# Kernel tuning notes

Measured on AMD Instinct MI355X. Metric: run time of the kernel, lower is better.

Reference implementation:

```python
import jax, jax.numpy as jnp
import numpy as np
from jax import lax

SEQ, BATCH, D_IN, HID = 2048, 16, 512, 512


def _qrnn_dir(X, W, b):
    # X: [S, B, D]; W: [3H, D]; b: [3H]
    g = jnp.einsum('sbd,hd->sbh', X, W) + b            # [S, B, 3H]
    z, f, o = jnp.split(g, 3, axis=-1)
    z = jnp.tanh(z)
    f = jax.nn.sigmoid(f)
    o = jax.nn.sigmoid(o)
    # fo-pooling recurrence: h_t = f_t*z_t + (1-f_t)*h_{t-1}, h_0 = 0
    # linear recurrence h_t = a_t*h_{t-1} + c_t with a = 1-f, c = f*z
    a = 1.0 - f
    c = f * z

    def combine(e1, e2):
        a1, c1 = e1
        a2, c2 = e2
        return (a1 * a2, a2 * c1 + c2)

    _, h = lax.associative_scan(combine, (a, c), axis=0)
    return o * h                                        # [S, B, H]


def setup_inputs() -> dict:
    key = jax.random.key(0)
    k = jax.random.split(key, 5)
    scale = 0.02
    return {
        'X': jax.random.normal(k[0], (SEQ, BATCH, D_IN), dtype=jnp.float32),
        'W_fw': jax.random.normal(k[1], (3 * HID, D_IN), dtype=jnp.float32) * scale,
        'b_fw': jnp.zeros((3 * HID,), dtype=jnp.float32),
        'W_bw': jax.random.normal(k[2], (3 * HID, D_IN), dtype=jnp.float32) * scale,
        'b_bw': jnp.zeros((3 * HID,), dtype=jnp.float32),
    }


def reference(X, W_fw, b_fw, W_bw, b_bw):
    Yfw = _qrnn_dir(X, W_fw, b_fw)                       # [S, B, H]
    Ybw = _qrnn_dir(jnp.flip(X, axis=0), W_bw, b_bw)     # [S, B, H]
    return jnp.concatenate((Yfw, jnp.flip(Ybw, axis=0)), axis=2)  # [S, B, 2H]
```

## Files before the change

kernel.cpp:

```cpp
#include <hip/hip_runtime.h>
#include <hip/hip_bf16.h>

#define SEQ   2048
#define BATCH 16
#define DIN   512
#define HID   512
#define MROWS (SEQ*BATCH)
#define NCOLS (6*HID)
#define KDIM  DIN

#define NC   32
#define CL   64
#define NSEQ (2*BATCH*HID)

typedef unsigned short u16;
typedef __bf16 bf16x8 __attribute__((ext_vector_type(8)));
typedef float  f32x4  __attribute__((ext_vector_type(4)));

__device__ __forceinline__ u16 f2bf(float x) {
  unsigned u = __float_as_uint(x);
  unsigned r = (u + 0x7fffu + ((u >> 16) & 1u)) >> 16;
  return (u16)r;
}
__device__ __forceinline__ float bflo(unsigned u) { return __uint_as_float(u << 16); }
__device__ __forceinline__ float bfhi(unsigned u) { return __uint_as_float(u & 0xffff0000u); }

__device__ __forceinline__ void async_ld16(const void* g, void* l) {
  __builtin_amdgcn_global_load_lds(
      (const __attribute__((address_space(1))) void*)g,
      (__attribute__((address_space(3))) void*)l, 16, 0, 0);
}

__device__ __forceinline__ float sig_fast(float x) {
  return __builtin_amdgcn_rcpf(1.f + __expf(-x));
}
__device__ __forceinline__ float tanh_fast(float x) {
  return 1.f - 2.f * __builtin_amdgcn_rcpf(1.f + __expf(2.f * x));
}

__global__ void cvt_kernel(const float* __restrict__ in, u16* __restrict__ out, int n4) {
  int i = blockIdx.x * blockDim.x + threadIdx.x;
  if (i >= n4) return;
  const float4 v = ((const float4*)in)[i];
  uint2 r;
  r.x = (unsigned)f2bf(v.x) | ((unsigned)f2bf(v.y) << 16);
  r.y = (unsigned)f2bf(v.z) | ((unsigned)f2bf(v.w) << 16);
  ((uint2*)out)[i] = r;
}

__launch_bounds__(256)
__global__ void gemm_gates(const u16* __restrict__ A, const u16* __restrict__ B,
                           const float* __restrict__ bfw, const float* __restrict__ bbw,
                           u16* __restrict__ G)
{
  __shared__ u16 sA[128 * 32];
  __shared__ u16 sB[128 * 32];

  const int t    = threadIdx.x;
  const int wave = t >> 6;
  const int lane = t & 63;
  const int m0 = blockIdx.y * 128;
  const int n0 = blockIdx.x * 128;
  const int wm = (wave >> 1) * 64;
  const int wn = (wave & 1) * 64;

  f32x4 acc[4][4] = {};

  const int srow = t >> 2;
  const int skcol = ((t & 3) ^ ((t >> 3) & 3)) * 8;
  const u16* gA = A + (size_t)(m0 + srow) * KDIM + skcol;
  const u16* gB = B + (size_t)(n0 + srow) * KDIM + skcol;
  u16* lA0 = sA + wave * 512;
  u16* lA1 = sA + 2048 + wave * 512;
  u16* lB0 = sB + wave * 512;
  u16* lB1 = sB + 2048 + wave * 512;

  const int lm  = lane & 15;
  const int q   = lane >> 4;
  const int swz = (lm >> 1) & 3;
  const int koff = ((q ^ swz) * 8);

  for (int kt = 0; kt < KDIM; kt += 32) {
    __syncthreads();
    async_ld16(gA + kt, lA0);
    async_ld16(gA + kt + (size_t)64 * KDIM, lA1);
    async_ld16(gB + kt, lB0);
    async_ld16(gB + kt + (size_t)64 * KDIM, lB1);
    __syncthreads();

    bf16x8 af[4], bfr[4];
#pragma unroll
    for (int mi = 0; mi < 4; mi++)
      af[mi] = *(const bf16x8*)(sA + (wm + mi * 16 + lm) * 32 + koff);
#pragma unroll
    for (int ni = 0; ni < 4; ni++)
      bfr[ni] = *(const bf16x8*)(sB + (wn + ni * 16 + lm) * 32 + koff);
#pragma unroll
    for (int mi = 0; mi < 4; mi++)
#pragma unroll
      for (int ni = 0; ni < 4; ni++)
        acc[mi][ni] = __builtin_amdgcn_mfma_f32_16x16x32_bf16(bfr[ni], af[mi], acc[mi][ni], 0, 0, 0);
  }

  const int q4 = q * 4;
#pragma unroll
  for (int ni = 0; ni < 4; ni++) {
    const int colb = n0 + wn + ni * 16 + q4;
    const int dir  = colb >= 1536 ? 1 : 0;
    const int rem  = colb - dir * 1536;
    const int gate = rem >> 9;
    const int hb   = rem & 511;
    const float4 bias4 = *(const float4*)((dir ? bbw : bfw) + rem);
    u16* Gs = G + (size_t)(dir * 3 + gate) * MROWS * HID + hb;
#pragma unroll
    for (int mi = 0; mi < 4; mi++) {
      const int m = m0 + wm + mi * 16 + lm;
      float v0 = acc[mi][ni][0] + bias4.x;
      float v1 = acc[mi][ni][1] + bias4.y;
      float v2 = acc[mi][ni][2] + bias4.z;
      float v3 = acc[mi][ni][3] + bias4.w;
      if (gate == 0) {
        v0 = tanh_fast(v0); v1 = tanh_fast(v1); v2 = tanh_fast(v2); v3 = tanh_fast(v3);
      } else {
        v0 = sig_fast(v0); v1 = sig_fast(v1); v2 = sig_fast(v2); v3 = sig_fast(v3);
      }
      uint2 pk;
      pk.x = (unsigned)f2bf(v0) | ((unsigned)f2bf(v1) << 16);
      pk.y = (unsigned)f2bf(v2) | ((unsigned)f2bf(v3) << 16);
      *(uint2*)(Gs + (size_t)m * HID) = pk;
    }
  }
}

__global__ void scan_stage1(const u16* __restrict__ G, float* __restrict__ AC) {
  const int tid = blockIdx.x * 256 + threadIdx.x;
  const int h     = (tid & 127) * 4;
  const int chunk = (tid >> 7) & 31;
  const int b     = (tid >> 12) & 15;
  const int dir   = tid >> 16;
  const u16* Zp = G + (size_t)(dir * 3 + 0) * MROWS * HID;
  const u16* Fp = G + (size_t)(dir * 3 + 1) * MROWS * HID;
  float A0 = 1.f, A1 = 1.f, A2 = 1.f, A3 = 1.f;
  float C0 = 0.f, C1 = 0.f, C2 = 0.f, C3 = 0.f;
  const int tbase = chunk * CL;
  for (int i = 0; i < CL; i++) {
    const int ts = tbase + i;
    const int s = dir ? (SEQ - 1 - ts) : ts;
    const size_t off = ((size_t)s * BATCH + b) * HID + h;
    const uint2 zu = *(const uint2*)(Zp + off);
    const uint2 fu = *(const uint2*)(Fp + off);
    const float z0 = bflo(zu.x), z1 = bfhi(zu.x), z2 = bflo(zu.y), z3 = bfhi(zu.y);
    const float f0 = bflo(fu.x), f1 = bfhi(fu.x), f2 = bflo(fu.y), f3 = bfhi(fu.y);
    const float a0 = 1.f - f0, a1 = 1.f - f1, a2 = 1.f - f2, a3 = 1.f - f3;
    C0 = fmaf(a0, C0, f0 * z0); A0 *= a0;
    C1 = fmaf(a1, C1, f1 * z1); A1 *= a1;
    C2 = fmaf(a2, C2, f2 * z2); A2 *= a2;
    C3 = fmaf(a3, C3, f3 * z3); A3 *= a3;
  }
  const int sidx = (dir * BATCH + b) * HID + h;
  *(float4*)&AC[(size_t)chunk * (2 * NSEQ) + sidx]        = make_float4(A0, A1, A2, A3);
  *(float4*)&AC[(size_t)chunk * (2 * NSEQ) + NSEQ + sidx] = make_float4(C0, C1, C2, C3);
}

__global__ void scan_stage2(const float* __restrict__ AC, float* __restrict__ Hin) {
  const int sidx = blockIdx.x * 256 + threadIdx.x;
  float carry = 0.f;
  for (int chunk = 0; chunk < NC; chunk++) {
    Hin[(size_t)chunk * NSEQ + sidx] = carry;
    const float Aa = AC[(size_t)chunk * (2 * NSEQ) + sidx];
    const float Cc = AC[(size_t)chunk * (2 * NSEQ) + NSEQ + sidx];
    carry = fmaf(Aa, carry, Cc);
  }
}

__global__ void scan_stage3(const u16* __restrict__ G, const float* __restrict__ Hin,
                            float* __restrict__ out) {
  const int tid = blockIdx.x * 256 + threadIdx.x;
  const int h     = (tid & 127) * 4;
  const int chunk = (tid >> 7) & 31;
  const int b     = (tid >> 12) & 15;
  const int dir   = tid >> 16;
  const u16* Zp = G + (size_t)(dir * 3 + 0) * MROWS * HID;
  const u16* Fp = G + (size_t)(dir * 3 + 1) * MROWS * HID;
  const u16* Op = G + (size_t)(dir * 3 + 2) * MROWS * HID;
  const int sidx = (dir * BATCH + b) * HID + h;
  float4 hv = *(const float4*)&Hin[(size_t)chunk * NSEQ + sidx];
  const int tbase = chunk * CL;
  for (int i = 0; i < CL; i++) {
    const int ts = tbase + i;
    const int s = dir ? (SEQ - 1 - ts) : ts;
    const size_t off = ((size_t)s * BATCH + b) * HID + h;
    const uint2 zu = *(const uint2*)(Zp + off);
    const uint2 fu = *(const uint2*)(Fp + off);
    const uint2 ou = *(const uint2*)(Op + off);
    const float z0 = bflo(zu.x), z1 = bfhi(zu.x), z2 = bflo(zu.y), z3 = bfhi(zu.y);
    const float f0 = bflo(fu.x), f1 = bfhi(fu.x), f2 = bflo(fu.y), f3 = bfhi(fu.y);
    hv.x = fmaf(f0, z0 - hv.x, hv.x);
    hv.y = fmaf(f1, z1 - hv.y, hv.y);
    hv.z = fmaf(f2, z2 - hv.z, hv.z);
    hv.w = fmaf(f3, z3 - hv.w, hv.w);
    float4 ov;
    ov.x = bflo(ou.x) * hv.x;
    ov.y = bfhi(ou.x) * hv.y;
    ov.z = bflo(ou.y) * hv.z;
    ov.w = bfhi(ou.y) * hv.w;
    *(float4*)&out[((size_t)s * BATCH + b) * (2 * HID) + (size_t)dir * HID + h] = ov;
  }
}

extern "C" void kernel_launch(void* const* d_in, const int* in_sizes, int n_in,
                              void* d_out, int out_size, void* d_ws, size_t ws_size,
                              hipStream_t stream) {
  const float* X   = (const float*)d_in[0];
  const float* Wfw = (const float*)d_in[1];
  const float* bfw = (const float*)d_in[2];
  const float* Wbw = (const float*)d_in[3];
  const float* bbw = (const float*)d_in[4];
  float* out = (float*)d_out;

  char* ws = (char*)d_ws;
  u16*   Xb  = (u16*)ws;
  u16*   Wb  = (u16*)(ws + (size_t)MROWS * KDIM * 2);
  u16*   G   = (u16*)(ws + (size_t)MROWS * KDIM * 2 + (size_t)NCOLS * KDIM * 2);
  float* AC  = (float*)((char*)G + (size_t)6 * MROWS * HID * 2);
  float* Hin = (float*)((char*)AC + (size_t)NC * 2 * NSEQ * 4);

  cvt_kernel<<<(MROWS * KDIM / 4) / 256, 256, 0, stream>>>(X, Xb, MROWS * KDIM / 4);
  cvt_kernel<<<(3 * HID * KDIM / 4) / 256, 256, 0, stream>>>(Wfw, Wb, 3 * HID * KDIM / 4);
  cvt_kernel<<<(3 * HID * KDIM / 4) / 256, 256, 0, stream>>>(Wbw, Wb + (size_t)3 * HID * KDIM,
                                                             3 * HID * KDIM / 4);

  dim3 gg(NCOLS / 128, MROWS / 128);
  gemm_gates<<<gg, 256, 0, stream>>>(Xb, Wb, bfw, bbw, G);

  scan_stage1<<<(NSEQ * NC / 4) / 256, 256, 0, stream>>>(G, AC);
  scan_stage2<<<NSEQ / 256, 256, 0, stream>>>(AC, Hin);
  scan_stage3<<<(NSEQ * NC / 4) / 256, 256, 0, stream>>>(G, Hin, out);
}
```

Measured before the change: 440.4 us.

## Deepen GEMM K-tile to 64 with XOR swizzle, halve scan chunks, nontemporal stores

The gate GEMM now stages a 64-wide K slice per iteration, using a new 8-way XOR swizzle for its LDS layout, and issues two MFMA sub-steps per barrier pair. This halves the number of sync points and doubles the shared memory per block. The scan uses 64 chunks of 32 steps to expose more parallelism, with an unroll pragma on its inner loops. Output stores become nontemporal to avoid cache pollution. Together these trade a longer serial carry pass in stage 2 and possibly lower occupancy for fewer barriers and better latency hiding.

```diff
diff --git a/kernel.cpp b/kernel.cpp
--- a/kernel.cpp
+++ b/kernel.cpp
@@ -9,8 +9,8 @@
 #define NCOLS (6*HID)
 #define KDIM  DIN
 
-#define NC   32
-#define CL   64
+#define NC   64
+#define CL   32
 #define NSEQ (2*BATCH*HID)
 
 typedef unsigned short u16;
@@ -53,8 +53,8 @@
                            const float* __restrict__ bfw, const float* __restrict__ bbw,
                            u16* __restrict__ G)
 {
-  __shared__ u16 sA[128 * 32];
-  __shared__ u16 sB[128 * 32];
+  __shared__ u16 sA[128 * 64];
+  __shared__ u16 sB[128 * 64];
 
   const int t    = threadIdx.x;
   const int wave = t >> 6;
@@ -66,40 +66,40 @@
 
   f32x4 acc[4][4] = {};
 
-  const int srow = t >> 2;
-  const int skcol = ((t & 3) ^ ((t >> 3) & 3)) * 8;
-  const u16* gA = A + (size_t)(m0 + srow) * KDIM + skcol;
-  const u16* gB = B + (size_t)(n0 + srow) * KDIM + skcol;
-  u16* lA0 = sA + wave * 512;
-  u16* lA1 = sA + 2048 + wave * 512;
-  u16* lB0 = sB + wave * 512;
-  u16* lB1 = sB + 2048 + wave * 512;
+  const int rloc = lane >> 3;
+  const int gch  = (lane & 7) ^ rloc;
+  const u16* gA = A + (size_t)(m0 + wave * 32 + rloc) * KDIM + gch * 8;
+  const u16* gB = B + (size_t)(n0 + wave * 32 + rloc) * KDIM + gch * 8;
 
   const int lm  = lane & 15;
   const int q   = lane >> 4;
-  const int swz = (lm >> 1) & 3;
-  const int koff = ((q ^ swz) * 8);
-
-  for (int kt = 0; kt < KDIM; kt += 32) {
+  const int xs  = lm & 7;
+
+  for (int kt = 0; kt < KDIM; kt += 64) {
     __syncthreads();
-    async_ld16(gA + kt, lA0);
-    async_ld16(gA + kt + (size_t)64 * KDIM, lA1);
-    async_ld16(gB + kt, lB0);
-    async_ld16(gB + kt + (size_t)64 * KDIM, lB1);
+#pragma unroll
+    for (int j = 0; j < 4; j++) {
+      async_ld16(gA + kt + (size_t)(j * 8) * KDIM, sA + (wave * 32 + j * 8) * 64);
+      async_ld16(gB + kt + (size_t)(j * 8) * KDIM, sB + (wave * 32 + j * 8) * 64);
+    }
     __syncthreads();
 
-    bf16x8 af[4], bfr[4];
-#pragma unroll
-    for (int mi = 0; mi < 4; mi++)
-      af[mi] = *(const bf16x8*)(sA + (wm + mi * 16 + lm) * 32 + koff);
-#pragma unroll
-    for (int ni = 0; ni < 4; ni++)
-      bfr[ni] = *(const bf16x8*)(sB + (wn + ni * 16 + lm) * 32 + koff);
-#pragma unroll
-    for (int mi = 0; mi < 4; mi++)
+#pragma unroll
+    for (int s = 0; s < 2; s++) {
+      const int cofs = ((s * 4 + q) ^ xs) * 8;
+      bf16x8 af[4], bfr[4];
+#pragma unroll
+      for (int mi = 0; mi < 4; mi++)
+        af[mi] = *(const bf16x8*)(sA + (wm + mi * 16 + lm) * 64 + cofs);
 #pragma unroll
       for (int ni = 0; ni < 4; ni++)
-        acc[mi][ni] = __builtin_amdgcn_mfma_f32_16x16x32_bf16(bfr[ni], af[mi], acc[mi][ni], 0, 0, 0);
+        bfr[ni] = *(const bf16x8*)(sB + (wn + ni * 16 + lm) * 64 + cofs);
+#pragma unroll
+      for (int mi = 0; mi < 4; mi++)
+#pragma unroll
+        for (int ni = 0; ni < 4; ni++)
+          acc[mi][ni] = __builtin_amdgcn_mfma_f32_16x16x32_bf16(bfr[ni], af[mi], acc[mi][ni], 0, 0, 0);
+    }
   }
 
   const int q4 = q * 4;
@@ -135,14 +135,15 @@
 __global__ void scan_stage1(const u16* __restrict__ G, float* __restrict__ AC) {
   const int tid = blockIdx.x * 256 + threadIdx.x;
   const int h     = (tid & 127) * 4;
-  const int chunk = (tid >> 7) & 31;
-  const int b     = (tid >> 12) & 15;
-  const int dir   = tid >> 16;
+  const int chunk = (tid >> 7) & 63;
+  const int b     = (tid >> 13) & 15;
+  const int dir   = tid >> 17;
   const u16* Zp = G + (size_t)(dir * 3 + 0) * MROWS * HID;
   const u16* Fp = G + (size_t)(dir * 3 + 1) * MROWS * HID;
   float A0 = 1.f, A1 = 1.f, A2 = 1.f, A3 = 1.f;
   float C0 = 0.f, C1 = 0.f, C2 = 0.f, C3 = 0.f;
   const int tbase = chunk * CL;
+#pragma unroll 8
   for (int i = 0; i < CL; i++) {
     const int ts = tbase + i;
     const int s = dir ? (SEQ - 1 - ts) : ts;
@@ -177,15 +178,16 @@
                             float* __restrict__ out) {
   const int tid = blockIdx.x * 256 + threadIdx.x;
   const int h     = (tid & 127) * 4;
-  const int chunk = (tid >> 7) & 31;
-  const int b     = (tid >> 12) & 15;
-  const int dir   = tid >> 16;
+  const int chunk = (tid >> 7) & 63;
+  const int b     = (tid >> 13) & 15;
+  const int dir   = tid >> 17;
   const u16* Zp = G + (size_t)(dir * 3 + 0) * MROWS * HID;
   const u16* Fp = G + (size_t)(dir * 3 + 1) * MROWS * HID;
   const u16* Op = G + (size_t)(dir * 3 + 2) * MROWS * HID;
   const int sidx = (dir * BATCH + b) * HID + h;
   float4 hv = *(const float4*)&Hin[(size_t)chunk * NSEQ + sidx];
   const int tbase = chunk * CL;
+#pragma unroll 8
   for (int i = 0; i < CL; i++) {
     const int ts = tbase + i;
     const int s = dir ? (SEQ - 1 - ts) : ts;
@@ -199,12 +201,13 @@
     hv.y = fmaf(f1, z1 - hv.y, hv.y);
     hv.z = fmaf(f2, z2 - hv.z, hv.z);
     hv.w = fmaf(f3, z3 - hv.w, hv.w);
-    float4 ov;
-    ov.x = bflo(ou.x) * hv.x;
-    ov.y = bfhi(ou.x) * hv.y;
-    ov.z = bflo(ou.y) * hv.z;
-    ov.w = bfhi(ou.y) * hv.w;
-    *(float4*)&out[((size_t)s * BATCH + b) * (2 * HID) + (size_t)dir * HID + h] = ov;
+    f32x4 ov;
+    ov[0] = bflo(ou.x) * hv.x;
+    ov[1] = bfhi(ou.x) * hv.y;
+    ov[2] = bflo(ou.y) * hv.z;
+    ov[3] = bfhi(ou.y) * hv.w;
+    __builtin_nontemporal_store(ov,
+        (f32x4*)&out[((size_t)s * BATCH + b) * (2 * HID) + (size_t)dir * HID + h]);
   }
 }
 
```

Measured after the change: 408.5 us. -7.2%, faster.
